# Performance work log

Measured on AMD Instinct MI355X. Metric: run time of the kernel, lower is better.

## Reference

```python
import jax, jax.numpy as jnp
import numpy as np

N_VARS = 4000
N_LITS = 2 * N_VARS
N_CLAUSES = 16000
N_CELLS = 48000
DIM = 128
N_ROUNDS = 16
N_PROBS = 8


def _mlp(x, w1, b1, w2, b2, w3, b3):
    x = jax.nn.relu(x @ w1.T + b1)
    x = jax.nn.relu(x @ w2.T + b2)
    return x @ w3.T + b3


def _lstm_step(x, h, c, wih, whh, bih, bhh):
    # PyTorch LSTM gate order: i, f, g, o
    gates = x @ wih.T + bih + h @ whh.T + bhh
    i, f, g, o = jnp.split(gates, 4, axis=-1)
    c = jax.nn.sigmoid(f) * c + jax.nn.sigmoid(i) * jnp.tanh(g)
    h = jax.nn.sigmoid(o) * jnp.tanh(c)
    return h, c


def setup_inputs() -> dict:
    key = jax.random.key(0)
    ks = iter(jax.random.split(key, 64))

    def p(shape, scale=0.05):
        return jax.random.normal(next(ks), shape, dtype=jnp.float32) * scale

    lit_idx = jax.random.randint(next(ks), (N_CELLS,), 0, N_LITS)
    cls_idx = jax.random.randint(next(ks), (N_CELLS,), 0, N_CLAUSES)
    L_unpack_indices = jnp.stack([lit_idx, cls_idx], axis=1)  # [n_cells, 2]

    return dict(
        L_unpack_indices=L_unpack_indices,
        n_vars=N_VARS, n_probs=N_PROBS, n_rounds=N_ROUNDS,
        L_init_w=p((DIM, 1)), L_init_b=p((DIM,)),
        C_init_w=p((DIM, 1)), C_init_b=p((DIM,)),
        Lmsg_w1=p((DIM, DIM)), Lmsg_b1=p((DIM,)),
        Lmsg_w2=p((DIM, DIM)), Lmsg_b2=p((DIM,)),
        Lmsg_w3=p((DIM, DIM)), Lmsg_b3=p((DIM,)),
        Cmsg_w1=p((DIM, DIM)), Cmsg_b1=p((DIM,)),
        Cmsg_w2=p((DIM, DIM)), Cmsg_b2=p((DIM,)),
        Cmsg_w3=p((DIM, DIM)), Cmsg_b3=p((DIM,)),
        Lvote_w1=p((DIM, DIM)), Lvote_b1=p((DIM,)),
        Lvote_w2=p((DIM, DIM)), Lvote_b2=p((DIM,)),
        Lvote_w3=p((1, DIM)), Lvote_b3=p((1,)),
        Lu_wih=p((4 * DIM, 2 * DIM)), Lu_whh=p((4 * DIM, DIM)),
        Lu_bih=p((4 * DIM,)), Lu_bhh=p((4 * DIM,)),
        Cu_wih=p((4 * DIM, DIM)), Cu_whh=p((4 * DIM, DIM)),
        Cu_bih=p((4 * DIM,)), Cu_bhh=p((4 * DIM,)),
    )


def reference(L_unpack_indices, n_vars, n_probs, n_rounds,
              L_init_w, L_init_b, C_init_w, C_init_b,
              Lmsg_w1, Lmsg_b1, Lmsg_w2, Lmsg_b2, Lmsg_w3, Lmsg_b3,
              Cmsg_w1, Cmsg_b1, Cmsg_w2, Cmsg_b2, Cmsg_w3, Cmsg_b3,
              Lvote_w1, Lvote_b1, Lvote_w2, Lvote_b2, Lvote_w3, Lvote_b3,
              Lu_wih, Lu_whh, Lu_bih, Lu_bhh,
              Cu_wih, Cu_whh, Cu_bih, Cu_bhh):
    n_lits = 2 * n_vars
    dim = L_init_b.shape[0]
    n_clauses = N_CLAUSES

    # densified literal-clause incidence matrix (matches torch.sparse -> to_dense)
    M = jnp.zeros((n_lits, n_clauses), jnp.float32).at[
        L_unpack_indices[:, 0], L_unpack_indices[:, 1]].add(1.0)

    # L_init/C_init applied to ts = ones(1)
    L0 = jnp.broadcast_to(L_init_w[:, 0] + L_init_b, (n_lits, dim))
    C0 = jnp.broadcast_to(C_init_w[:, 0] + C_init_b, (n_clauses, dim))
    carry0 = (L0, jnp.zeros((n_lits, dim), jnp.float32),
              C0, jnp.zeros((n_clauses, dim), jnp.float32))

    def round_fn(carry, _):
        Lh, Lc, Ch, Cc = carry
        L_pre = _mlp(Lh, Lmsg_w1, Lmsg_b1, Lmsg_w2, Lmsg_b2, Lmsg_w3, Lmsg_b3)
        LC_msg = M.T @ L_pre                      # [n_clauses, dim]
        Ch, Cc = _lstm_step(LC_msg, Ch, Cc, Cu_wih, Cu_whh, Cu_bih, Cu_bhh)
        C_pre = _mlp(Ch, Cmsg_w1, Cmsg_b1, Cmsg_w2, Cmsg_b2, Cmsg_w3, Cmsg_b3)
        CL_msg = M @ C_pre                        # [n_lits, dim]
        flipped = jnp.concatenate([Lh[n_vars:2 * n_vars], Lh[:n_vars]], axis=0)
        Lh, Lc = _lstm_step(jnp.concatenate([CL_msg, flipped], axis=1),
                            Lh, Lc, Lu_wih, Lu_whh, Lu_bih, Lu_bhh)
        return (Lh, Lc, Ch, Cc), None

    (Lh, _, _, _), _ = jax.lax.scan(round_fn, carry0, None, length=n_rounds)

    vote = _mlp(Lh, Lvote_w1, Lvote_b1, Lvote_w2, Lvote_b2, Lvote_w3, Lvote_b3)  # [n_lits, 1]
    vote_join = jnp.concatenate([vote[:n_vars], vote[n_vars:]], axis=1)          # [n_vars, 2]
    vote_join = vote_join.reshape(n_probs, -1)
    return jnp.mean(vote_join, axis=1)
```

## Files before the change

kernel.cpp:

```cpp
#include <hip/hip_runtime.h>
#include <cstdint>
#include <cstddef>

#define N_VARS   4000
#define N_LITS   8000
#define N_CLAUSES 16000
#define N_CELLS  48000
#define DIM      128
#define N_ROUNDS 16
#define N_PROBS  8

typedef __bf16 bf16x8 __attribute__((ext_vector_type(8)));
typedef float f32x4 __attribute__((ext_vector_type(4)));

__device__ inline unsigned short f2bf(float x) {
  unsigned int u = __float_as_uint(x);
  u += 0x7fffu + ((u >> 16) & 1u);
  return (unsigned short)(u >> 16);
}
__device__ inline float bflo(unsigned int v) { return __uint_as_float(v << 16); }
__device__ inline float bfhi(unsigned int v) { return __uint_as_float(v & 0xffff0000u); }
__device__ inline unsigned int pack2(float a, float b) {
  return (unsigned int)f2bf(a) | ((unsigned int)f2bf(b) << 16);
}
__device__ inline bf16x8 ld_frag(const unsigned short* p) {
  uint4 u = *reinterpret_cast<const uint4*>(p);
  return __builtin_bit_cast(bf16x8, u);
}
__device__ inline float fast_sigmoid(float x) { return 1.f / (1.f + __expf(-x)); }
__device__ inline float fast_tanh(float x) {
  float t = __expf(-2.f * x);
  return (1.f - t) / (1.f + t);
}


template<int KS, bool LIT>
__global__ __launch_bounds__(512, 4) void fused_round(
    const int* __restrict__ ptr, const int* __restrict__ col,
    const unsigned short* __restrict__ Tsrc,
    const unsigned short* hold, unsigned short* hnew,
    float* __restrict__ cst,
    const unsigned short* __restrict__ Wp, const float* __restrict__ bP,
    const unsigned short* __restrict__ Wm1, const float* __restrict__ bm1,
    const unsigned short* __restrict__ Wm2, const float* __restrict__ bm2,
    const unsigned short* __restrict__ Wm3, const float* __restrict__ bm3,
    unsigned short* __restrict__ Tout) {
  __shared__ __align__(16) unsigned short msg[32][136];
  __shared__ __align__(16) unsigned short hsA[32][136];
  __shared__ __align__(16) unsigned short hsF[LIT ? 32 : 1][136];
  __shared__ __align__(16) unsigned short xb[32][136];
  const int tid = threadIdx.x;
  const int w = tid >> 6, l = tid & 63;
  const int r = l & 15, kc = l >> 4;
  const int row0 = blockIdx.x * 32;
  const int flipoff = LIT ? ((row0 < N_VARS) ? N_VARS : -N_VARS) : 0;

  float s[16];
  {
    const int g8 = tid >> 3, gl = tid & 7;
    const int grow = g8 & 31, part = g8 >> 5;
    const int row = row0 + grow;
    const int b = ptr[row], e = ptr[row + 1];
#pragma unroll
    for (int q = 0; q < 16; ++q) s[q] = 0.f;
    int j = b + part;
    int c0 = (j < e) ? col[j] : 0;
    while (j < e) {
      const int jn = j + 2;
      const int c1 = (jn < e) ? col[jn] : 0;
      const unsigned short* src = &Tsrc[(size_t)c0 * 128 + gl * 16];
      const uint4 v0 = *reinterpret_cast<const uint4*>(src);
      const uint4 v1 = *reinterpret_cast<const uint4*>(src + 8);
      s[0]  += bflo(v0.x); s[1]  += bfhi(v0.x);
      s[2]  += bflo(v0.y); s[3]  += bfhi(v0.y);
      s[4]  += bflo(v0.z); s[5]  += bfhi(v0.z);
      s[6]  += bflo(v0.w); s[7]  += bfhi(v0.w);
      s[8]  += bflo(v1.x); s[9]  += bfhi(v1.x);
      s[10] += bflo(v1.y); s[11] += bfhi(v1.y);
      s[12] += bflo(v1.z); s[13] += bfhi(v1.z);
      s[14] += bflo(v1.w); s[15] += bfhi(v1.w);
      j = jn; c0 = c1;
    }
    if (part == 1) {
      uint4 o0, o1;
      o0.x = pack2(s[0], s[1]);  o0.y = pack2(s[2], s[3]);
      o0.z = pack2(s[4], s[5]);  o0.w = pack2(s[6], s[7]);
      o1.x = pack2(s[8], s[9]);  o1.y = pack2(s[10], s[11]);
      o1.z = pack2(s[12], s[13]); o1.w = pack2(s[14], s[15]);
      *reinterpret_cast<uint4*>(&msg[grow][gl * 16]) = o0;
      *reinterpret_cast<uint4*>(&msg[grow][gl * 16 + 8]) = o1;
    }
  }
  __syncthreads();

  {
    const int g8 = tid >> 3, gl = tid & 7;
    const int grow = g8 & 31, part = g8 >> 5;
    if (part == 0) {
      const uint4 m0 = *reinterpret_cast<const uint4*>(&msg[grow][gl * 16]);
      const uint4 m1 = *reinterpret_cast<const uint4*>(&msg[grow][gl * 16 + 8]);
      s[0]  += bflo(m0.x); s[1]  += bfhi(m0.x);
      s[2]  += bflo(m0.y); s[3]  += bfhi(m0.y);
      s[4]  += bflo(m0.z); s[5]  += bfhi(m0.z);
      s[6]  += bflo(m0.w); s[7]  += bfhi(m0.w);
      s[8]  += bflo(m1.x); s[9]  += bfhi(m1.x);
      s[10] += bflo(m1.y); s[11] += bfhi(m1.y);
      s[12] += bflo(m1.z); s[13] += bfhi(m1.z);
      s[14] += bflo(m1.w); s[15] += bfhi(m1.w);
      uint4 o0, o1;
      o0.x = pack2(s[0], s[1]);  o0.y = pack2(s[2], s[3]);
      o0.z = pack2(s[4], s[5]);  o0.w = pack2(s[6], s[7]);
      o1.x = pack2(s[8], s[9]);  o1.y = pack2(s[10], s[11]);
      o1.z = pack2(s[12], s[13]); o1.w = pack2(s[14], s[15]);
      *reinterpret_cast<uint4*>(&msg[grow][gl * 16]) = o0;
      *reinterpret_cast<uint4*>(&msg[grow][gl * 16 + 8]) = o1;
    } else {
      const int sidx = tid - 256;
#pragma unroll
      for (int q = 0; q < 2; ++q) {
        const int n = sidx + q * 256;
        const int rw = n >> 4, c8 = (n & 15) * 8;
        *reinterpret_cast<uint4*>(&hsA[rw][c8]) =
            *reinterpret_cast<const uint4*>(&hold[(size_t)(row0 + rw) * 128 + c8]);
        if (LIT)
          *reinterpret_cast<uint4*>(&hsF[rw][c8]) =
              *reinterpret_cast<const uint4*>(&hold[(size_t)(row0 + flipoff + rw) * 128 + c8]);
      }
    }
  }
  __syncthreads();

  f32x4 acc[2][4];
#pragma unroll
  for (int rg = 0; rg < 2; ++rg)
#pragma unroll
    for (int t = 0; t < 4; ++t) acc[rg][t] = (f32x4){0.f, 0.f, 0.f, 0.f};

#pragma unroll
  for (int ks = 0; ks < KS; ++ks) {
    bf16x8 bfr[2];
#pragma unroll
    for (int rg = 0; rg < 2; ++rg) {
      const int xr = rg * 16 + r;
      if (ks < 4)        bfr[rg] = ld_frag(&msg[xr][ks * 32 + kc * 8]);
      else if (!LIT)     bfr[rg] = ld_frag(&hsA[xr][(ks - 4) * 32 + kc * 8]);
      else if (ks < 8)   bfr[rg] = ld_frag(&hsF[xr][(ks - 4) * 32 + kc * 8]);
      else               bfr[rg] = ld_frag(&hsA[xr][(ks - 8) * 32 + kc * 8]);
    }
#pragma unroll
    for (int tt = 0; tt < 4; ++tt) {
      bf16x8 afr = ld_frag(&Wp[(size_t)(((w * KS + ks) * 4 + tt) * 64 + l) * 8]);
      acc[0][tt] = __builtin_amdgcn_mfma_f32_16x16x32_bf16(afr, bfr[0], acc[0][tt], 0, 0, 0);
      acc[1][tt] = __builtin_amdgcn_mfma_f32_16x16x32_bf16(afr, bfr[1], acc[1][tt], 0, 0, 0);
    }
  }
  __syncthreads();

  {
    const int d0 = w * 16 + kc * 4;
#pragma unroll
    for (int rg = 0; rg < 2; ++rg) {
      const int row = row0 + rg * 16 + r;
      const size_t cb = (size_t)row * 128 + d0;
      f32x4 cv = *reinterpret_cast<const f32x4*>(&cst[cb]);
      f32x4 cn4;
      unsigned int hp[2];
#pragma unroll
      for (int tt = 0; tt < 4; ++tt) {
        const float4 bb = *reinterpret_cast<const float4*>(&bP[w * 64 + tt * 16 + kc * 4]);
        float ig = acc[rg][tt][0] + bb.x;
        float fg = acc[rg][tt][1] + bb.y;
        float gg = acc[rg][tt][2] + bb.z;
        float og = acc[rg][tt][3] + bb.w;
        float cn = fast_sigmoid(fg) * cv[tt] + fast_sigmoid(ig) * fast_tanh(gg);
        float hv = fast_sigmoid(og) * fast_tanh(cn);
        cn4[tt] = cn;
        if (tt & 1) hp[tt >> 1] |= (unsigned int)f2bf(hv) << 16;
        else        hp[tt >> 1]  = (unsigned int)f2bf(hv);
      }
      *reinterpret_cast<f32x4*>(&cst[cb]) = cn4;
      uint2 hv2 = {hp[0], hp[1]};
      *reinterpret_cast<uint2*>(&hnew[cb]) = hv2;
      *reinterpret_cast<uint2*>(&hsA[rg * 16 + r][d0]) = hv2;
    }
  }
  __syncthreads();

  const int mrg = w >> 2;
  const int t0 = (w & 3) * 2;
  {
    f32x4 a2[2] = {(f32x4){0.f, 0.f, 0.f, 0.f}, (f32x4){0.f, 0.f, 0.f, 0.f}};
#pragma unroll
    for (int ks = 0; ks < 4; ++ks) {
      bf16x8 af = ld_frag(&hsA[mrg * 16 + r][ks * 32 + kc * 8]);
#pragma unroll
      for (int q = 0; q < 2; ++q) {
        bf16x8 bf = ld_frag(&Wm1[(size_t)(((t0 + q) * 4 + ks) * 64 + l) * 8]);
        a2[q] = __builtin_amdgcn_mfma_f32_16x16x32_bf16(af, bf, a2[q], 0, 0, 0);
      }
    }
#pragma unroll
    for (int q = 0; q < 2; ++q) {
      float bv = bm1[(t0 + q) * 16 + r];
#pragma unroll
      for (int j = 0; j < 4; ++j)
        xb[mrg * 16 + kc * 4 + j][(t0 + q) * 16 + r] = f2bf(fmaxf(a2[q][j] + bv, 0.f));
    }
  }
  __syncthreads();
  {
    f32x4 a2[2] = {(f32x4){0.f, 0.f, 0.f, 0.f}, (f32x4){0.f, 0.f, 0.f, 0.f}};
#pragma unroll
    for (int ks = 0; ks < 4; ++ks) {
      bf16x8 af = ld_frag(&xb[mrg * 16 + r][ks * 32 + kc * 8]);
#pragma unroll
      for (int q = 0; q < 2; ++q) {
        bf16x8 bf = ld_frag(&Wm2[(size_t)(((t0 + q) * 4 + ks) * 64 + l) * 8]);
        a2[q] = __builtin_amdgcn_mfma_f32_16x16x32_bf16(af, bf, a2[q], 0, 0, 0);
      }
    }
#pragma unroll
    for (int q = 0; q < 2; ++q) {
      float bv = bm2[(t0 + q) * 16 + r];
#pragma unroll
      for (int j = 0; j < 4; ++j)
        msg[mrg * 16 + kc * 4 + j][(t0 + q) * 16 + r] = f2bf(fmaxf(a2[q][j] + bv, 0.f));
    }
  }
  __syncthreads();
  {
    f32x4 a2[2] = {(f32x4){0.f, 0.f, 0.f, 0.f}, (f32x4){0.f, 0.f, 0.f, 0.f}};
#pragma unroll
    for (int ks = 0; ks < 4; ++ks) {
      bf16x8 af = ld_frag(&msg[mrg * 16 + r][ks * 32 + kc * 8]);
#pragma unroll
      for (int q = 0; q < 2; ++q) {
        bf16x8 bf = ld_frag(&Wm3[(size_t)(((t0 + q) * 4 + ks) * 64 + l) * 8]);
        a2[q] = __builtin_amdgcn_mfma_f32_16x16x32_bf16(af, bf, a2[q], 0, 0, 0);
      }
    }
#pragma unroll
    for (int q = 0; q < 2; ++q) {
      float bv = bm3[(t0 + q) * 16 + r];
#pragma unroll
      for (int j = 0; j < 4; ++j)
        Tout[(size_t)(row0 + mrg * 16 + kc * 4 + j) * 128 + (t0 + q) * 16 + r] =
            f2bf(a2[q][j] + bv);
    }
  }
}

__global__ __launch_bounds__(256) void fused_mlp3(
    const unsigned short* __restrict__ A,
    const unsigned short* __restrict__ W1, const float* __restrict__ b1,
    const unsigned short* __restrict__ W2, const float* __restrict__ b2,
    const unsigned short* __restrict__ W3, const float* __restrict__ b3,
    unsigned short* __restrict__ out) {
  __shared__ __align__(16) unsigned short xbuf[2][4][16][136];
  const int w = threadIdx.x >> 6, l = threadIdx.x & 63;
  const int r = l & 15, kc = l >> 4;
  const int row0 = blockIdx.x * 64 + w * 16;

  f32x4 acc[8];
#pragma unroll
  for (int t = 0; t < 8; ++t) acc[t] = (f32x4){0.f, 0.f, 0.f, 0.f};
#pragma unroll
  for (int ks = 0; ks < 4; ++ks) {
    bf16x8 a = ld_frag(&A[(size_t)(row0 + r) * 128 + ks * 32 + kc * 8]);
#pragma unroll
    for (int t = 0; t < 8; ++t) {
      bf16x8 b = ld_frag(&W1[(size_t)((t * 4 + ks) * 64 + l) * 8]);
      acc[t] = __builtin_amdgcn_mfma_f32_16x16x32_bf16(a, b, acc[t], 0, 0, 0);
    }
  }
#pragma unroll
  for (int t = 0; t < 8; ++t) {
    float bv = b1[t * 16 + r];
#pragma unroll
    for (int j = 0; j < 4; ++j)
      xbuf[0][w][kc * 4 + j][t * 16 + r] = f2bf(fmaxf(acc[t][j] + bv, 0.f));
  }
// ... 113 lines not shown
__global__ void pack8_kernel(const float* s0, const float* s1, const float* s2, const float* s3,
                             const float* s4, const float* s5, const float* s6, const float* s7,
                             unsigned short* d0, unsigned short* d1, unsigned short* d2,
                             unsigned short* d3, unsigned short* d4, unsigned short* d5,
                             unsigned short* d6, unsigned short* d7) {
  int i = blockIdx.x * 256 + threadIdx.x;
  const float* s; unsigned short* d;
  switch (blockIdx.y) {
    case 0: s = s0; d = d0; break;
    case 1: s = s1; d = d1; break;
    case 2: s = s2; d = d2; break;
    case 3: s = s3; d = d3; break;
    case 4: s = s4; d = d4; break;
    case 5: s = s5; d = d5; break;
    case 6: s = s6; d = d6; break;
    default: s = s7; d = d7; break;
  }
  int np = i >> 7, k = i & 127;
  int tt = np >> 4, r = np & 15;
  int ks = k >> 5, kcf = (k >> 3) & 3, e = k & 7;
  int dst = (((tt * 4 + ks) * 64) + kcf * 16 + r) * 8 + e;
  d[dst] = f2bf(s[i]);
}

template<int KIH>
__global__ void pack_gates_kernel(const float* __restrict__ wih, const float* __restrict__ whh,
                                  const float* __restrict__ bih, const float* __restrict__ bhh,
                                  unsigned short* __restrict__ Wp, float* __restrict__ bP) {
  constexpr int K = KIH + 128;
  constexpr int KS = K / 32;
  int idx = blockIdx.x * 256 + threadIdx.x;
  if (idx >= 512 * K) return;
  int np = idx / K, k = idx % K;
  int gt = np & 3;
  int d = ((np >> 6) << 4) + (((np >> 2) & 3) << 2) + ((np >> 4) & 3);
  int orig = gt * 128 + d;
  float v = (k < KIH) ? wih[(size_t)orig * KIH + k] : whh[(size_t)orig * 128 + (k - KIH)];
  int w = np >> 6, tt = (np >> 4) & 3, r = np & 15;
  int ks = k >> 5, kcf = (k >> 3) & 3, e = k & 7;
  size_t dst = ((size_t)((w * KS + ks) * 4 + tt) * 64 + kcf * 16 + r) * 8 + e;
  Wp[dst] = f2bf(v);
  if (k == 0) bP[np] = bih[orig] + bhh[orig];
}

__global__ void count_kernel(const int* __restrict__ uidx,
                             int* __restrict__ lit_cnt, int* __restrict__ cls_cnt) {
  int i = blockIdx.x * 256 + threadIdx.x;
  if (i < N_CELLS) {
    atomicAdd(&lit_cnt[uidx[2 * i]], 1);
    atomicAdd(&cls_cnt[uidx[2 * i + 1]], 1);
  }
}

__global__ void scan_kernel(const int* __restrict__ cnt, int* __restrict__ ptr, int n) {
  __shared__ int part[1024];
  __shared__ int total;
  int t = threadIdx.x;
  int chunk = (n + 1023) >> 10;
  int lo = t * chunk, hi = min(lo + chunk, n);
  int s = 0;
  for (int i = lo; i < hi; ++i) s += cnt[i];
  part[t] = s;
  __syncthreads();
  if (t == 0) {
    int acc = 0;
    for (int i = 0; i < 1024; ++i) { int v = part[i]; part[i] = acc; acc += v; }
    total = acc;
  }
  __syncthreads();
  int acc = part[t];
  for (int i = lo; i < hi; ++i) { ptr[i] = acc; acc += cnt[i]; }
  if (t == 0) ptr[n] = total;
}
// ... 80 lines not shown
  unsigned short* wV2  = (unsigned short*)alloc(DIM * DIM * 2);
  int* lit_cnt  = (int*)alloc(N_LITS * 4);
  int* cls_cnt  = (int*)alloc(N_CLAUSES * 4);
  int* lit_fill = (int*)alloc(N_LITS * 4);
  int* cls_fill = (int*)alloc(N_CLAUSES * 4);
  int* lit_ptr  = (int*)alloc((N_LITS + 1) * 4);
  int* cls_ptr  = (int*)alloc((N_CLAUSES + 1) * 4);
  int* lit_col  = (int*)alloc(N_CELLS * 4);
  int* cls_col  = (int*)alloc(N_CELLS * 4);
  if (off > ws_size) return;

  hipMemsetAsync(lit_cnt, 0, (char*)lit_ptr - (char*)lit_cnt, stream);
  count_kernel<<<(N_CELLS + 255) / 256, 256, 0, stream>>>(uidx, lit_cnt, cls_cnt);
  scan_kernel<<<1, 1024, 0, stream>>>(lit_cnt, lit_ptr, N_LITS);
  scan_kernel<<<1, 1024, 0, stream>>>(cls_cnt, cls_ptr, N_CLAUSES);
  scatter_kernel<<<(N_CELLS + 255) / 256, 256, 0, stream>>>(
      uidx, lit_ptr, cls_ptr, lit_fill, cls_fill, lit_col, cls_col);

  init_state_kernel<<<(N_CLAUSES * DIM + 255) / 256, 256, 0, stream>>>(
      L_init_w, L_init_b, C_init_w, C_init_b, LhA, Lc, Ch, Cc);
  pack_gates_kernel<256><<<(512 * 384 + 255) / 256, 256, 0, stream>>>(
      Lu_wih, Lu_whh, Lu_bih, Lu_bhh, WLp, bL);
  pack_gates_kernel<128><<<(512 * 256 + 255) / 256, 256, 0, stream>>>(
      Cu_wih, Cu_whh, Cu_bih, Cu_bhh, WCp, bC);
  dim3 cgrid(DIM * DIM / 256, 8);
  pack8_kernel<<<cgrid, 256, 0, stream>>>(
      Lmsg_w1, Lmsg_w2, Lmsg_w3, Cmsg_w1, Cmsg_w2, Cmsg_w3, Lvote_w1, Lvote_w2,
      wLm1, wLm2, wLm3, wCm1, wCm2, wCm3, wV1, wV2);

  fused_mlp3<<<N_LITS / 64, 256, 0, stream>>>(
      LhA, wLm1, Lmsg_b1, wLm2, Lmsg_b2, wLm3, Lmsg_b3, TL);

  for (int r = 0; r < N_ROUNDS; ++r) {
    fused_round<8, false><<<N_CLAUSES / 32, 512, 0, stream>>>(
        cls_ptr, cls_col, TL, Ch, Ch, Cc, WCp, bC,
        wCm1, Cmsg_b1, wCm2, Cmsg_b2, wCm3, Cmsg_b3, TC);
    const unsigned short* lold = (r & 1) ? LhB : LhA;
    unsigned short* lnew = (r & 1) ? LhA : LhB;
    fused_round<12, true><<<N_LITS / 32, 512, 0, stream>>>(
        lit_ptr, lit_col, TC, lold, lnew, Lc, WLp, bL,
        wLm1, Lmsg_b1, wLm2, Lmsg_b2, wLm3, Lmsg_b3, TL);
  }

  fused_vote<<<N_LITS / 64, 256, 0, stream>>>(
      LhA, wV1, Lvote_b1, wV2, Lvote_b2, Lvote_w3, Lvote_b3, vote);
  prob_mean_kernel<<<N_PROBS, 256, 0, stream>>>(vote, out);
}
```

Baseline: 715.7 us.

## Double fused_round block to 1024 threads and prefetch hidden state early

Each per-round fused kernel now uses 1024 threads (16 waves) per 32-row tile instead of 512. The gather uses 16 lanes per row with 8 elements each, each wave computes half as many gate tiles, and each MLP wave produces one output tile. The gate weight packing is reordered to match. The old hidden-state rows are loaded into registers at kernel start so their latency overlaps the sparse gather. This is meant to raise parallelism and latency hiding, at the cost of scalar (non-vectorised) cell-state and hidden writes, more waves per block and an extra barrier.

```diff
diff --git a/kernel.cpp b/kernel.cpp
--- a/kernel.cpp
+++ b/kernel.cpp
@@ -35,7 +35,7 @@
 
 
 template<int KS, bool LIT>
-__global__ __launch_bounds__(512, 4) void fused_round(
+__global__ __launch_bounds__(1024, 8) void fused_round(
     const int* __restrict__ ptr, const int* __restrict__ col,
     const unsigned short* __restrict__ Tsrc,
     const unsigned short* hold, unsigned short* hnew,
@@ -53,88 +53,74 @@
   const int w = tid >> 6, l = tid & 63;
   const int r = l & 15, kc = l >> 4;
   const int row0 = blockIdx.x * 32;
-  const int flipoff = LIT ? ((row0 < N_VARS) ? N_VARS : -N_VARS) : 0;
-
-  float s[16];
+
+  uint4 stA, stF;
+  if (tid >= 512) {
+    const int sidx = tid - 512;
+    const int rw = sidx >> 4, c8 = (sidx & 15) * 8;
+    stA = *reinterpret_cast<const uint4*>(&hold[(size_t)(row0 + rw) * 128 + c8]);
+    if (LIT) {
+      const int gr = row0 + rw;
+      const int fr = (gr < N_VARS) ? gr + N_VARS : gr - N_VARS;
+      stF = *reinterpret_cast<const uint4*>(&hold[(size_t)fr * 128 + c8]);
+    }
+  }
+
+  float s[8];
   {
-    const int g8 = tid >> 3, gl = tid & 7;
-    const int grow = g8 & 31, part = g8 >> 5;
+    const int g16 = tid >> 4, gl = tid & 15;
+    const int grow = g16 & 31, part = g16 >> 5;
     const int row = row0 + grow;
     const int b = ptr[row], e = ptr[row + 1];
 #pragma unroll
-    for (int q = 0; q < 16; ++q) s[q] = 0.f;
+    for (int q = 0; q < 8; ++q) s[q] = 0.f;
     int j = b + part;
     int c0 = (j < e) ? col[j] : 0;
     while (j < e) {
       const int jn = j + 2;
       const int c1 = (jn < e) ? col[jn] : 0;
-      const unsigned short* src = &Tsrc[(size_t)c0 * 128 + gl * 16];
-      const uint4 v0 = *reinterpret_cast<const uint4*>(src);
-      const uint4 v1 = *reinterpret_cast<const uint4*>(src + 8);
-      s[0]  += bflo(v0.x); s[1]  += bfhi(v0.x);
-      s[2]  += bflo(v0.y); s[3]  += bfhi(v0.y);
-      s[4]  += bflo(v0.z); s[5]  += bfhi(v0.z);
-      s[6]  += bflo(v0.w); s[7]  += bfhi(v0.w);
-      s[8]  += bflo(v1.x); s[9]  += bfhi(v1.x);
-      s[10] += bflo(v1.y); s[11] += bfhi(v1.y);
-      s[12] += bflo(v1.z); s[13] += bfhi(v1.z);
-      s[14] += bflo(v1.w); s[15] += bfhi(v1.w);
+      const uint4 v = *reinterpret_cast<const uint4*>(&Tsrc[(size_t)c0 * 128 + gl * 8]);
+      s[0] += bflo(v.x); s[1] += bfhi(v.x);
+      s[2] += bflo(v.y); s[3] += bfhi(v.y);
+      s[4] += bflo(v.z); s[5] += bfhi(v.z);
+      s[6] += bflo(v.w); s[7] += bfhi(v.w);
       j = jn; c0 = c1;
     }
     if (part == 1) {
-      uint4 o0, o1;
-      o0.x = pack2(s[0], s[1]);  o0.y = pack2(s[2], s[3]);
-      o0.z = pack2(s[4], s[5]);  o0.w = pack2(s[6], s[7]);
-      o1.x = pack2(s[8], s[9]);  o1.y = pack2(s[10], s[11]);
-      o1.z = pack2(s[12], s[13]); o1.w = pack2(s[14], s[15]);
-      *reinterpret_cast<uint4*>(&msg[grow][gl * 16]) = o0;
-      *reinterpret_cast<uint4*>(&msg[grow][gl * 16 + 8]) = o1;
+      uint4 o;
+      o.x = pack2(s[0], s[1]); o.y = pack2(s[2], s[3]);
+      o.z = pack2(s[4], s[5]); o.w = pack2(s[6], s[7]);
+      *reinterpret_cast<uint4*>(&msg[grow][gl * 8]) = o;
     }
   }
   __syncthreads();
 
   {
-    const int g8 = tid >> 3, gl = tid & 7;
-    const int grow = g8 & 31, part = g8 >> 5;
+    const int g16 = tid >> 4, gl = tid & 15;
+    const int grow = g16 & 31, part = g16 >> 5;
     if (part == 0) {
-      const uint4 m0 = *reinterpret_cast<const uint4*>(&msg[grow][gl * 16]);
-      const uint4 m1 = *reinterpret_cast<const uint4*>(&msg[grow][gl * 16 + 8]);
-      s[0]  += bflo(m0.x); s[1]  += bfhi(m0.x);
-      s[2]  += bflo(m0.y); s[3]  += bfhi(m0.y);
-      s[4]  += bflo(m0.z); s[5]  += bfhi(m0.z);
-      s[6]  += bflo(m0.w); s[7]  += bfhi(m0.w);
-      s[8]  += bflo(m1.x); s[9]  += bfhi(m1.x);
-      s[10] += bflo(m1.y); s[11] += bfhi(m1.y);
-      s[12] += bflo(m1.z); s[13] += bfhi(m1.z);
-      s[14] += bflo(m1.w); s[15] += bfhi(m1.w);
-      uint4 o0, o1;
-      o0.x = pack2(s[0], s[1]);  o0.y = pack2(s[2], s[3]);
-      o0.z = pack2(s[4], s[5]);  o0.w = pack2(s[6], s[7]);
-      o1.x = pack2(s[8], s[9]);  o1.y = pack2(s[10], s[11]);
-      o1.z = pack2(s[12], s[13]); o1.w = pack2(s[14], s[15]);
-      *reinterpret_cast<uint4*>(&msg[grow][gl * 16]) = o0;
-      *reinterpret_cast<uint4*>(&msg[grow][gl * 16 + 8]) = o1;
+      const uint4 m = *reinterpret_cast<const uint4*>(&msg[grow][gl * 8]);
+      uint4 o;
+      o.x = pack2(s[0] + bflo(m.x), s[1] + bfhi(m.x));
+      o.y = pack2(s[2] + bflo(m.y), s[3] + bfhi(m.y));
+      o.z = pack2(s[4] + bflo(m.z), s[5] + bfhi(m.z));
+      o.w = pack2(s[6] + bflo(m.w), s[7] + bfhi(m.w));
+      *reinterpret_cast<uint4*>(&msg[grow][gl * 8]) = o;
     } else {
-      const int sidx = tid - 256;
-#pragma unroll
-      for (int q = 0; q < 2; ++q) {
-        const int n = sidx + q * 256;
-        const int rw = n >> 4, c8 = (n & 15) * 8;
-        *reinterpret_cast<uint4*>(&hsA[rw][c8]) =
-            *reinterpret_cast<const uint4*>(&hold[(size_t)(row0 + rw) * 128 + c8]);
-        if (LIT)
-          *reinterpret_cast<uint4*>(&hsF[rw][c8]) =
-              *reinterpret_cast<const uint4*>(&hold[(size_t)(row0 + flipoff + rw) * 128 + c8]);
-      }
-    }
-  }
-  __syncthreads();
-
-  f32x4 acc[2][4];
+      const int sidx = tid - 512;
+      const int rw = sidx >> 4, c8 = (sidx & 15) * 8;
+      *reinterpret_cast<uint4*>(&hsA[rw][c8]) = stA;
+      if (LIT)
+        *reinterpret_cast<uint4*>(&hsF[rw][c8]) = stF;
+    }
+  }
+  __syncthreads();
+
+  f32x4 acc[2][2];
 #pragma unroll
   for (int rg = 0; rg < 2; ++rg)
 #pragma unroll
-    for (int t = 0; t < 4; ++t) acc[rg][t] = (f32x4){0.f, 0.f, 0.f, 0.f};
+    for (int t = 0; t < 2; ++t) acc[rg][t] = (f32x4){0.f, 0.f, 0.f, 0.f};
 
 #pragma unroll
   for (int ks = 0; ks < KS; ++ks) {
@@ -148,8 +134,8 @@
       else               bfr[rg] = ld_frag(&hsA[xr][(ks - 8) * 32 + kc * 8]);
     }
 #pragma unroll
-    for (int tt = 0; tt < 4; ++tt) {
-      bf16x8 afr = ld_frag(&Wp[(size_t)(((w * KS + ks) * 4 + tt) * 64 + l) * 8]);
+    for (int tt = 0; tt < 2; ++tt) {
+      bf16x8 afr = ld_frag(&Wp[(size_t)(((w * KS + ks) * 2 + tt) * 64 + l) * 8]);
       acc[0][tt] = __builtin_amdgcn_mfma_f32_16x16x32_bf16(afr, bfr[0], acc[0][tt], 0, 0, 0);
       acc[1][tt] = __builtin_amdgcn_mfma_f32_16x16x32_bf16(afr, bfr[1], acc[1][tt], 0, 0, 0);
     }
@@ -157,96 +143,74 @@
   __syncthreads();
 
   {
-    const int d0 = w * 16 + kc * 4;
 #pragma unroll
     for (int rg = 0; rg < 2; ++rg) {
       const int row = row0 + rg * 16 + r;
-      const size_t cb = (size_t)row * 128 + d0;
-      f32x4 cv = *reinterpret_cast<const f32x4*>(&cst[cb]);
-      f32x4 cn4;
-      unsigned int hp[2];
-#pragma unroll
-      for (int tt = 0; tt < 4; ++tt) {
-        const float4 bb = *reinterpret_cast<const float4*>(&bP[w * 64 + tt * 16 + kc * 4]);
+#pragma unroll
+      for (int tt = 0; tt < 2; ++tt) {
+        const int d = w * 8 + tt * 4 + kc;
+        const size_t cb = (size_t)row * 128 + d;
+        const float4 bb = *reinterpret_cast<const float4*>(&bP[w * 32 + tt * 16 + kc * 4]);
         float ig = acc[rg][tt][0] + bb.x;
         float fg = acc[rg][tt][1] + bb.y;
         float gg = acc[rg][tt][2] + bb.z;
         float og = acc[rg][tt][3] + bb.w;
-        float cn = fast_sigmoid(fg) * cv[tt] + fast_sigmoid(ig) * fast_tanh(gg);
+        float cp = cst[cb];
+        float cn = fast_sigmoid(fg) * cp + fast_sigmoid(ig) * fast_tanh(gg);
         float hv = fast_sigmoid(og) * fast_tanh(cn);
-        cn4[tt] = cn;
-        if (tt & 1) hp[tt >> 1] |= (unsigned int)f2bf(hv) << 16;
-        else        hp[tt >> 1]  = (unsigned int)f2bf(hv);
+        cst[cb] = cn;
+        unsigned short hb16 = f2bf(hv);
+        hnew[cb] = hb16;
+        hsA[rg * 16 + r][d] = hb16;
       }
-      *reinterpret_cast<f32x4*>(&cst[cb]) = cn4;
-      uint2 hv2 = {hp[0], hp[1]};
-      *reinterpret_cast<uint2*>(&hnew[cb]) = hv2;
-      *reinterpret_cast<uint2*>(&hsA[rg * 16 + r][d0]) = hv2;
-    }
-  }
-  __syncthreads();
-
-  const int mrg = w >> 2;
-  const int t0 = (w & 3) * 2;
+    }
+  }
+  __syncthreads();
+
+  const int mrg = w >> 3;
+  const int t0 = w & 7;
   {
-    f32x4 a2[2] = {(f32x4){0.f, 0.f, 0.f, 0.f}, (f32x4){0.f, 0.f, 0.f, 0.f}};
+    f32x4 a2 = (f32x4){0.f, 0.f, 0.f, 0.f};
 #pragma unroll
     for (int ks = 0; ks < 4; ++ks) {
       bf16x8 af = ld_frag(&hsA[mrg * 16 + r][ks * 32 + kc * 8]);
-#pragma unroll
-      for (int q = 0; q < 2; ++q) {
-        bf16x8 bf = ld_frag(&Wm1[(size_t)(((t0 + q) * 4 + ks) * 64 + l) * 8]);
-        a2[q] = __builtin_amdgcn_mfma_f32_16x16x32_bf16(af, bf, a2[q], 0, 0, 0);
-      }
-    }
-#pragma unroll
-    for (int q = 0; q < 2; ++q) {
-      float bv = bm1[(t0 + q) * 16 + r];
-#pragma unroll
-      for (int j = 0; j < 4; ++j)
-        xb[mrg * 16 + kc * 4 + j][(t0 + q) * 16 + r] = f2bf(fmaxf(a2[q][j] + bv, 0.f));
-    }
+      bf16x8 bf = ld_frag(&Wm1[(size_t)((t0 * 4 + ks) * 64 + l) * 8]);
+      a2 = __builtin_amdgcn_mfma_f32_16x16x32_bf16(af, bf, a2, 0, 0, 0);
+    }
+    float bv = bm1[t0 * 16 + r];
+#pragma unroll
+    for (int j = 0; j < 4; ++j)
+      xb[mrg * 16 + kc * 4 + j][t0 * 16 + r] = f2bf(fmaxf(a2[j] + bv, 0.f));
   }
   __syncthreads();
   {
-    f32x4 a2[2] = {(f32x4){0.f, 0.f, 0.f, 0.f}, (f32x4){0.f, 0.f, 0.f, 0.f}};
+    f32x4 a2 = (f32x4){0.f, 0.f, 0.f, 0.f};
 #pragma unroll
     for (int ks = 0; ks < 4; ++ks) {
       bf16x8 af = ld_frag(&xb[mrg * 16 + r][ks * 32 + kc * 8]);
-#pragma unroll
-      for (int q = 0; q < 2; ++q) {
-        bf16x8 bf = ld_frag(&Wm2[(size_t)(((t0 + q) * 4 + ks) * 64 + l) * 8]);
-        a2[q] = __builtin_amdgcn_mfma_f32_16x16x32_bf16(af, bf, a2[q], 0, 0, 0);
-      }
-    }
-#pragma unroll
-    for (int q = 0; q < 2; ++q) {
-      float bv = bm2[(t0 + q) * 16 + r];
-#pragma unroll
-      for (int j = 0; j < 4; ++j)
-        msg[mrg * 16 + kc * 4 + j][(t0 + q) * 16 + r] = f2bf(fmaxf(a2[q][j] + bv, 0.f));
-    }
+      bf16x8 bf = ld_frag(&Wm2[(size_t)((t0 * 4 + ks) * 64 + l) * 8]);
+      a2 = __builtin_amdgcn_mfma_f32_16x16x32_bf16(af, bf, a2, 0, 0, 0);
+    }
+    float bv = bm2[t0 * 16 + r];
+    __syncthreads();
+#pragma unroll
+    for (int j = 0; j < 4; ++j)
+      msg[mrg * 16 + kc * 4 + j][t0 * 16 + r] = f2bf(fmaxf(a2[j] + bv, 0.f));
   }
   __syncthreads();
   {
-    f32x4 a2[2] = {(f32x4){0.f, 0.f, 0.f, 0.f}, (f32x4){0.f, 0.f, 0.f, 0.f}};
+    f32x4 a2 = (f32x4){0.f, 0.f, 0.f, 0.f};
 #pragma unroll
     for (int ks = 0; ks < 4; ++ks) {
       bf16x8 af = ld_frag(&msg[mrg * 16 + r][ks * 32 + kc * 8]);
-#pragma unroll
-      for (int q = 0; q < 2; ++q) {
-        bf16x8 bf = ld_frag(&Wm3[(size_t)(((t0 + q) * 4 + ks) * 64 + l) * 8]);
-        a2[q] = __builtin_amdgcn_mfma_f32_16x16x32_bf16(af, bf, a2[q], 0, 0, 0);
-      }
-    }
-#pragma unroll
-    for (int q = 0; q < 2; ++q) {
-      float bv = bm3[(t0 + q) * 16 + r];
-#pragma unroll
-      for (int j = 0; j < 4; ++j)
-        Tout[(size_t)(row0 + mrg * 16 + kc * 4 + j) * 128 + (t0 + q) * 16 + r] =
-            f2bf(a2[q][j] + bv);
-    }
+      bf16x8 bf = ld_frag(&Wm3[(size_t)((t0 * 4 + ks) * 64 + l) * 8]);
+      a2 = __builtin_amdgcn_mfma_f32_16x16x32_bf16(af, bf, a2, 0, 0, 0);
+    }
+    float bv = bm3[t0 * 16 + r];
+#pragma unroll
+    for (int j = 0; j < 4; ++j)
+      Tout[(size_t)(row0 + mrg * 16 + kc * 4 + j) * 128 + t0 * 16 + r] =
+          f2bf(a2[j] + bv);
   }
 }
 
@@ -427,12 +391,12 @@
   if (idx >= 512 * K) return;
   int np = idx / K, k = idx % K;
   int gt = np & 3;
-  int d = ((np >> 6) << 4) + (((np >> 2) & 3) << 2) + ((np >> 4) & 3);
+  int d = ((np >> 5) << 3) + (((np >> 4) & 1) << 2) + ((np >> 2) & 3);
   int orig = gt * 128 + d;
   float v = (k < KIH) ? wih[(size_t)orig * KIH + k] : whh[(size_t)orig * 128 + (k - KIH)];
-  int w = np >> 6, tt = (np >> 4) & 3, r = np & 15;
+  int w = np >> 5, tt = (np >> 4) & 1, rr = np & 15;
   int ks = k >> 5, kcf = (k >> 3) & 3, e = k & 7;
-  size_t dst = ((size_t)((w * KS + ks) * 4 + tt) * 64 + kcf * 16 + r) * 8 + e;
+  size_t dst = ((size_t)((w * KS + ks) * 2 + tt) * 64 + kcf * 16 + rr) * 8 + e;
   Wp[dst] = f2bf(v);
   if (k == 0) bP[np] = bih[orig] + bhh[orig];
 }
@@ -579,12 +543,12 @@
       LhA, wLm1, Lmsg_b1, wLm2, Lmsg_b2, wLm3, Lmsg_b3, TL);
 
   for (int r = 0; r < N_ROUNDS; ++r) {
-    fused_round<8, false><<<N_CLAUSES / 32, 512, 0, stream>>>(
+    fused_round<8, false><<<N_CLAUSES / 32, 1024, 0, stream>>>(
         cls_ptr, cls_col, TL, Ch, Ch, Cc, WCp, bC,
         wCm1, Cmsg_b1, wCm2, Cmsg_b2, wCm3, Cmsg_b3, TC);
     const unsigned short* lold = (r & 1) ? LhB : LhA;
     unsigned short* lnew = (r & 1) ? LhA : LhB;
-    fused_round<12, true><<<N_LITS / 32, 512, 0, stream>>>(
+    fused_round<12, true><<<N_LITS / 32, 1024, 0, stream>>>(
         lit_ptr, lit_col, TC, lold, lnew, Lc, WLp, bL,
         wLm1, Lmsg_b1, wLm2, Lmsg_b2, wLm3, Lmsg_b3, TL);
   }
```

Measured after the change: 818.4 us. 14.4% more time.

## Halve literal-round tile to 16 rows and prefetch hidden state before gather

Applied to the files above, without the earlier changes.

Adds an RG template parameter so the literal-side round kernel processes 16 rows per block, doubling the block count to 500 for better CU coverage. The gather is split into four partial sums per row, reduced through a small shared buffer. The old hidden state and its flipped counterpart are loaded into registers before the sparse gather so their latency overlaps with it. The trade-off is half the MFMA work per weight fragment load in the literal kernel, so weight traffic per row roughly doubles.

```diff
diff --git a/kernel.cpp b/kernel.cpp
--- a/kernel.cpp
+++ b/kernel.cpp
@@ -34,7 +34,7 @@
 }
 
 
-template<int KS, bool LIT>
+template<int KS, int RG, bool LIT>
 __global__ __launch_bounds__(512, 4) void fused_round(
     const int* __restrict__ ptr, const int* __restrict__ col,
     const unsigned short* __restrict__ Tsrc,
@@ -45,20 +45,39 @@
     const unsigned short* __restrict__ Wm2, const float* __restrict__ bm2,
     const unsigned short* __restrict__ Wm3, const float* __restrict__ bm3,
     unsigned short* __restrict__ Tout) {
-  __shared__ __align__(16) unsigned short msg[32][136];
-  __shared__ __align__(16) unsigned short hsA[32][136];
-  __shared__ __align__(16) unsigned short hsF[LIT ? 32 : 1][136];
-  __shared__ __align__(16) unsigned short xb[32][136];
+  constexpr int ROWS = RG * 16;
+  __shared__ __align__(16) unsigned short msg[ROWS][136];
+  __shared__ __align__(16) unsigned short hsA[ROWS][136];
+  __shared__ __align__(16) unsigned short hsF[LIT ? ROWS : 1][136];
+  __shared__ __align__(16) unsigned short xb[ROWS][136];
+  __shared__ __align__(16) unsigned short pmsg[RG == 1 ? 3 : 1][RG == 1 ? 16 : 1][136];
   const int tid = threadIdx.x;
   const int w = tid >> 6, l = tid & 63;
   const int r = l & 15, kc = l >> 4;
-  const int row0 = blockIdx.x * 32;
-  const int flipoff = LIT ? ((row0 < N_VARS) ? N_VARS : -N_VARS) : 0;
+  const int row0 = blockIdx.x * ROWS;
+
+  uint4 stA[2], stF[2];
+  if (tid >= 256) {
+    const int sidx = tid - 256;
+#pragma unroll
+    for (int q = 0; q < RG; ++q) {
+      const int n = sidx + q * 256;
+      const int rw = n >> 4, c8 = (n & 15) * 8;
+      stA[q] = *reinterpret_cast<const uint4*>(&hold[(size_t)(row0 + rw) * 128 + c8]);
+      if (LIT) {
+        const int gr = row0 + rw;
+        const int fr = (gr < N_VARS) ? gr + N_VARS : gr - N_VARS;
+        stF[q] = *reinterpret_cast<const uint4*>(&hold[(size_t)fr * 128 + c8]);
+      }
+    }
+  }
 
   float s[16];
   {
     const int g8 = tid >> 3, gl = tid & 7;
-    const int grow = g8 & 31, part = g8 >> 5;
+    const int grow = (RG == 2) ? (g8 & 31) : (g8 & 15);
+    const int part = (RG == 2) ? (g8 >> 5) : (g8 >> 4);
+    constexpr int NPART = (RG == 2) ? 2 : 4;
     const int row = row0 + grow;
     const int b = ptr[row], e = ptr[row + 1];
 #pragma unroll
@@ -66,7 +85,7 @@
     int j = b + part;
     int c0 = (j < e) ? col[j] : 0;
     while (j < e) {
-      const int jn = j + 2;
+      const int jn = j + NPART;
       const int c1 = (jn < e) ? col[jn] : 0;
       const unsigned short* src = &Tsrc[(size_t)c0 * 128 + gl * 16];
       const uint4 v0 = *reinterpret_cast<const uint4*>(src);
@@ -81,7 +100,51 @@
       s[14] += bflo(v1.w); s[15] += bfhi(v1.w);
       j = jn; c0 = c1;
     }
-    if (part == 1) {
+    if (part > 0) {
+      uint4 o0, o1;
+      o0.x = pack2(s[0], s[1]);  o0.y = pack2(s[2], s[3]);
+      o0.z = pack2(s[4], s[5]);  o0.w = pack2(s[6], s[7]);
+      o1.x = pack2(s[8], s[9]);  o1.y = pack2(s[10], s[11]);
+      o1.z = pack2(s[12], s[13]); o1.w = pack2(s[14], s[15]);
+      unsigned short* dst = (RG == 2) ? &msg[grow][gl * 16]
+                                      : &pmsg[part - 1][grow][gl * 16];
+      *reinterpret_cast<uint4*>(dst) = o0;
+      *reinterpret_cast<uint4*>(dst + 8) = o1;
+    }
+  }
+  __syncthreads();
+
+  {
+    const int g8 = tid >> 3, gl = tid & 7;
+    const int grow = (RG == 2) ? (g8 & 31) : (g8 & 15);
+    const int part = (RG == 2) ? (g8 >> 5) : (g8 >> 4);
+    if (part == 0) {
+      if (RG == 2) {
+        const uint4 m0 = *reinterpret_cast<const uint4*>(&msg[grow][gl * 16]);
+        const uint4 m1 = *reinterpret_cast<const uint4*>(&msg[grow][gl * 16 + 8]);
+        s[0]  += bflo(m0.x); s[1]  += bfhi(m0.x);
+        s[2]  += bflo(m0.y); s[3]  += bfhi(m0.y);
+        s[4]  += bflo(m0.z); s[5]  += bfhi(m0.z);
+        s[6]  += bflo(m0.w); s[7]  += bfhi(m0.w);
+        s[8]  += bflo(m1.x); s[9]  += bfhi(m1.x);
+        s[10] += bflo(m1.y); s[11] += bfhi(m1.y);
+        s[12] += bflo(m1.z); s[13] += bfhi(m1.z);
+        s[14] += bflo(m1.w); s[15] += bfhi(m1.w);
+      } else {
+#pragma unroll
+        for (int p = 0; p < 3; ++p) {
+          const uint4 m0 = *reinterpret_cast<const uint4*>(&pmsg[p][grow][gl * 16]);
+          const uint4 m1 = *reinterpret_cast<const uint4*>(&pmsg[p][grow][gl * 16 + 8]);
+          s[0]  += bflo(m0.x); s[1]  += bfhi(m0.x);
+          s[2]  += bflo(m0.y); s[3]  += bfhi(m0.y);
+          s[4]  += bflo(m0.z); s[5]  += bfhi(m0.z);
+          s[6]  += bflo(m0.w); s[7]  += bfhi(m0.w);
+          s[8]  += bflo(m1.x); s[9]  += bfhi(m1.x);
+          s[10] += bflo(m1.y); s[11] += bfhi(m1.y);
+          s[12] += bflo(m1.z); s[13] += bfhi(m1.z);
+          s[14] += bflo(m1.w); s[15] += bfhi(m1.w);
+        }
+      }
       uint4 o0, o1;
       o0.x = pack2(s[0], s[1]);  o0.y = pack2(s[2], s[3]);
       o0.z = pack2(s[4], s[5]);  o0.w = pack2(s[6], s[7]);
@@ -89,58 +152,31 @@
       o1.z = pack2(s[12], s[13]); o1.w = pack2(s[14], s[15]);
       *reinterpret_cast<uint4*>(&msg[grow][gl * 16]) = o0;
       *reinterpret_cast<uint4*>(&msg[grow][gl * 16 + 8]) = o1;
-    }
-  }
-  __syncthreads();
-
-  {
-    const int g8 = tid >> 3, gl = tid & 7;
-    const int grow = g8 & 31, part = g8 >> 5;
-    if (part == 0) {
-      const uint4 m0 = *reinterpret_cast<const uint4*>(&msg[grow][gl * 16]);
-      const uint4 m1 = *reinterpret_cast<const uint4*>(&msg[grow][gl * 16 + 8]);
-      s[0]  += bflo(m0.x); s[1]  += bfhi(m0.x);
-      s[2]  += bflo(m0.y); s[3]  += bfhi(m0.y);
-      s[4]  += bflo(m0.z); s[5]  += bfhi(m0.z);
-      s[6]  += bflo(m0.w); s[7]  += bfhi(m0.w);
-      s[8]  += bflo(m1.x); s[9]  += bfhi(m1.x);
-      s[10] += bflo(m1.y); s[11] += bfhi(m1.y);
-      s[12] += bflo(m1.z); s[13] += bfhi(m1.z);
-      s[14] += bflo(m1.w); s[15] += bfhi(m1.w);
-      uint4 o0, o1;
-      o0.x = pack2(s[0], s[1]);  o0.y = pack2(s[2], s[3]);
-      o0.z = pack2(s[4], s[5]);  o0.w = pack2(s[6], s[7]);
-      o1.x = pack2(s[8], s[9]);  o1.y = pack2(s[10], s[11]);
-      o1.z = pack2(s[12], s[13]); o1.w = pack2(s[14], s[15]);
-      *reinterpret_cast<uint4*>(&msg[grow][gl * 16]) = o0;
-      *reinterpret_cast<uint4*>(&msg[grow][gl * 16 + 8]) = o1;
-    } else {
+    } else if (tid >= 256) {
       const int sidx = tid - 256;
 #pragma unroll
-      for (int q = 0; q < 2; ++q) {
+      for (int q = 0; q < RG; ++q) {
         const int n = sidx + q * 256;
         const int rw = n >> 4, c8 = (n & 15) * 8;
-        *reinterpret_cast<uint4*>(&hsA[rw][c8]) =
-            *reinterpret_cast<const uint4*>(&hold[(size_t)(row0 + rw) * 128 + c8]);
+        *reinterpret_cast<uint4*>(&hsA[rw][c8]) = stA[q];
         if (LIT)
-          *reinterpret_cast<uint4*>(&hsF[rw][c8]) =
-              *reinterpret_cast<const uint4*>(&hold[(size_t)(row0 + flipoff + rw) * 128 + c8]);
+          *reinterpret_cast<uint4*>(&hsF[rw][c8]) = stF[q];
       }
     }
   }
   __syncthreads();
 
-  f32x4 acc[2][4];
-#pragma unroll
-  for (int rg = 0; rg < 2; ++rg)
+  f32x4 acc[RG][4];
+#pragma unroll
+  for (int rg = 0; rg < RG; ++rg)
 #pragma unroll
     for (int t = 0; t < 4; ++t) acc[rg][t] = (f32x4){0.f, 0.f, 0.f, 0.f};
 
 #pragma unroll
   for (int ks = 0; ks < KS; ++ks) {
-    bf16x8 bfr[2];
-#pragma unroll
-    for (int rg = 0; rg < 2; ++rg) {
+    bf16x8 bfr[RG];
+#pragma unroll
+    for (int rg = 0; rg < RG; ++rg) {
       const int xr = rg * 16 + r;
       if (ks < 4)        bfr[rg] = ld_frag(&msg[xr][ks * 32 + kc * 8]);
       else if (!LIT)     bfr[rg] = ld_frag(&hsA[xr][(ks - 4) * 32 + kc * 8]);
@@ -150,8 +186,9 @@
 #pragma unroll
     for (int tt = 0; tt < 4; ++tt) {
       bf16x8 afr = ld_frag(&Wp[(size_t)(((w * KS + ks) * 4 + tt) * 64 + l) * 8]);
-      acc[0][tt] = __builtin_amdgcn_mfma_f32_16x16x32_bf16(afr, bfr[0], acc[0][tt], 0, 0, 0);
-      acc[1][tt] = __builtin_amdgcn_mfma_f32_16x16x32_bf16(afr, bfr[1], acc[1][tt], 0, 0, 0);
+#pragma unroll
+      for (int rg = 0; rg < RG; ++rg)
+        acc[rg][tt] = __builtin_amdgcn_mfma_f32_16x16x32_bf16(afr, bfr[rg], acc[rg][tt], 0, 0, 0);
     }
   }
   __syncthreads();
@@ -159,7 +196,7 @@
   {
     const int d0 = w * 16 + kc * 4;
 #pragma unroll
-    for (int rg = 0; rg < 2; ++rg) {
+    for (int rg = 0; rg < RG; ++rg) {
       const int row = row0 + rg * 16 + r;
       const size_t cb = (size_t)row * 128 + d0;
       f32x4 cv = *reinterpret_cast<const f32x4*>(&cst[cb]);
@@ -186,21 +223,24 @@
   }
   __syncthreads();
 
-  const int mrg = w >> 2;
-  const int t0 = (w & 3) * 2;
+  constexpr int TPW = (RG == 2) ? 2 : 1;
+  const int mrg = (RG == 2) ? (w >> 2) : 0;
+  const int t0 = (RG == 2) ? ((w & 3) * 2) : w;
   {
-    f32x4 a2[2] = {(f32x4){0.f, 0.f, 0.f, 0.f}, (f32x4){0.f, 0.f, 0.f, 0.f}};
+    f32x4 a2[TPW];
+#pragma unroll
+    for (int q = 0; q < TPW; ++q) a2[q] = (f32x4){0.f, 0.f, 0.f, 0.f};
 #pragma unroll
     for (int ks = 0; ks < 4; ++ks) {
       bf16x8 af = ld_frag(&hsA[mrg * 16 + r][ks * 32 + kc * 8]);
 #pragma unroll
-      for (int q = 0; q < 2; ++q) {
+      for (int q = 0; q < TPW; ++q) {
         bf16x8 bf = ld_frag(&Wm1[(size_t)(((t0 + q) * 4 + ks) * 64 + l) * 8]);
         a2[q] = __builtin_amdgcn_mfma_f32_16x16x32_bf16(af, bf, a2[q], 0, 0, 0);
       }
     }
 #pragma unroll
-    for (int q = 0; q < 2; ++q) {
+    for (int q = 0; q < TPW; ++q) {
       float bv = bm1[(t0 + q) * 16 + r];
 #pragma unroll
       for (int j = 0; j < 4; ++j)
@@ -209,18 +249,20 @@
   }
   __syncthreads();
   {
-    f32x4 a2[2] = {(f32x4){0.f, 0.f, 0.f, 0.f}, (f32x4){0.f, 0.f, 0.f, 0.f}};
+    f32x4 a2[TPW];
+#pragma unroll
+    for (int q = 0; q < TPW; ++q) a2[q] = (f32x4){0.f, 0.f, 0.f, 0.f};
 #pragma unroll
     for (int ks = 0; ks < 4; ++ks) {
       bf16x8 af = ld_frag(&xb[mrg * 16 + r][ks * 32 + kc * 8]);
 #pragma unroll
-      for (int q = 0; q < 2; ++q) {
+      for (int q = 0; q < TPW; ++q) {
         bf16x8 bf = ld_frag(&Wm2[(size_t)(((t0 + q) * 4 + ks) * 64 + l) * 8]);
         a2[q] = __builtin_amdgcn_mfma_f32_16x16x32_bf16(af, bf, a2[q], 0, 0, 0);
       }
     }
 #pragma unroll
-    for (int q = 0; q < 2; ++q) {
+    for (int q = 0; q < TPW; ++q) {
       float bv = bm2[(t0 + q) * 16 + r];
 #pragma unroll
       for (int j = 0; j < 4; ++j)
@@ -229,18 +271,20 @@
   }
   __syncthreads();
   {
-    f32x4 a2[2] = {(f32x4){0.f, 0.f, 0.f, 0.f}, (f32x4){0.f, 0.f, 0.f, 0.f}};
+    f32x4 a2[TPW];
+#pragma unroll
+    for (int q = 0; q < TPW; ++q) a2[q] = (f32x4){0.f, 0.f, 0.f, 0.f};
 #pragma unroll
     for (int ks = 0; ks < 4; ++ks) {
       bf16x8 af = ld_frag(&msg[mrg * 16 + r][ks * 32 + kc * 8]);
 #pragma unroll
-      for (int q = 0; q < 2; ++q) {
+      for (int q = 0; q < TPW; ++q) {
         bf16x8 bf = ld_frag(&Wm3[(size_t)(((t0 + q) * 4 + ks) * 64 + l) * 8]);
         a2[q] = __builtin_amdgcn_mfma_f32_16x16x32_bf16(af, bf, a2[q], 0, 0, 0);
       }
     }
 #pragma unroll
-    for (int q = 0; q < 2; ++q) {
+    for (int q = 0; q < TPW; ++q) {
       float bv = bm3[(t0 + q) * 16 + r];
 #pragma unroll
       for (int j = 0; j < 4; ++j)
@@ -430,9 +474,9 @@
   int d = ((np >> 6) << 4) + (((np >> 2) & 3) << 2) + ((np >> 4) & 3);
   int orig = gt * 128 + d;
   float v = (k < KIH) ? wih[(size_t)orig * KIH + k] : whh[(size_t)orig * 128 + (k - KIH)];
-  int w = np >> 6, tt = (np >> 4) & 3, r = np & 15;
+  int w = np >> 6, tt = (np >> 4) & 3, rr = np & 15;
   int ks = k >> 5, kcf = (k >> 3) & 3, e = k & 7;
-  size_t dst = ((size_t)((w * KS + ks) * 4 + tt) * 64 + kcf * 16 + r) * 8 + e;
+  size_t dst = ((size_t)((w * KS + ks) * 4 + tt) * 64 + kcf * 16 + rr) * 8 + e;
   Wp[dst] = f2bf(v);
   if (k == 0) bP[np] = bih[orig] + bhh[orig];
 }
@@ -579,12 +623,12 @@
       LhA, wLm1, Lmsg_b1, wLm2, Lmsg_b2, wLm3, Lmsg_b3, TL);
 
   for (int r = 0; r < N_ROUNDS; ++r) {
-    fused_round<8, false><<<N_CLAUSES / 32, 512, 0, stream>>>(
+    fused_round<8, 2, false><<<N_CLAUSES / 32, 512, 0, stream>>>(
         cls_ptr, cls_col, TL, Ch, Ch, Cc, WCp, bC,
         wCm1, Cmsg_b1, wCm2, Cmsg_b2, wCm3, Cmsg_b3, TC);
     const unsigned short* lold = (r & 1) ? LhB : LhA;
     unsigned short* lnew = (r & 1) ? LhA : LhB;
-    fused_round<12, true><<<N_LITS / 32, 512, 0, stream>>>(
+    fused_round<12, 1, true><<<N_LITS / 16, 512, 0, stream>>>(
         lit_ptr, lit_col, TC, lold, lnew, Lc, WLp, bL,
         wLm1, Lmsg_b1, wLm2, Lmsg_b2, wLm3, Lmsg_b3, TL);
   }
```

Measured after the change: 715.4 us. About the same (-0.0%).

## Retile LSTM gate GEMM per wave and prefetch hidden state before gather

Applied to the files above, without the earlier changes.

Each wave now computes 8 gate tiles (128 gate outputs) for one 16-row half instead of 4 tiles for both row halves. The gate weight packing is reordered so each thread owns 8 contiguous hidden dims, which gives 16-byte cell-state and h stores. The hidden-state and flipped-state global loads are issued into registers before the sparse gather loop, so their latency overlaps the gather. Each wave now reads twice as much weight data from global memory per block but only one B fragment per k-step, and register pressure rises.

```diff
diff --git a/kernel.cpp b/kernel.cpp
--- a/kernel.cpp
+++ b/kernel.cpp
@@ -53,7 +53,22 @@
   const int w = tid >> 6, l = tid & 63;
   const int r = l & 15, kc = l >> 4;
   const int row0 = blockIdx.x * 32;
-  const int flipoff = LIT ? ((row0 < N_VARS) ? N_VARS : -N_VARS) : 0;
+
+  uint4 stA[2], stF[2];
+  if (tid >= 256) {
+    const int sidx = tid - 256;
+#pragma unroll
+    for (int q = 0; q < 2; ++q) {
+      const int n = sidx + q * 256;
+      const int rw = n >> 4, c8 = (n & 15) * 8;
+      stA[q] = *reinterpret_cast<const uint4*>(&hold[(size_t)(row0 + rw) * 128 + c8]);
+      if (LIT) {
+        const int gr = row0 + rw;
+        const int fr = (gr < N_VARS) ? gr + N_VARS : gr - N_VARS;
+        stF[q] = *reinterpret_cast<const uint4*>(&hold[(size_t)fr * 128 + c8]);
+      }
+    }
+  }
 
   float s[16];
   {
@@ -114,75 +129,71 @@
       o1.z = pack2(s[12], s[13]); o1.w = pack2(s[14], s[15]);
       *reinterpret_cast<uint4*>(&msg[grow][gl * 16]) = o0;
       *reinterpret_cast<uint4*>(&msg[grow][gl * 16 + 8]) = o1;
-    } else {
+    } else if (tid >= 256) {
       const int sidx = tid - 256;
 #pragma unroll
       for (int q = 0; q < 2; ++q) {
         const int n = sidx + q * 256;
         const int rw = n >> 4, c8 = (n & 15) * 8;
-        *reinterpret_cast<uint4*>(&hsA[rw][c8]) =
-            *reinterpret_cast<const uint4*>(&hold[(size_t)(row0 + rw) * 128 + c8]);
+        *reinterpret_cast<uint4*>(&hsA[rw][c8]) = stA[q];
         if (LIT)
-          *reinterpret_cast<uint4*>(&hsF[rw][c8]) =
-              *reinterpret_cast<const uint4*>(&hold[(size_t)(row0 + flipoff + rw) * 128 + c8]);
+          *reinterpret_cast<uint4*>(&hsF[rw][c8]) = stF[q];
       }
     }
   }
   __syncthreads();
 
-  f32x4 acc[2][4];
-#pragma unroll
-  for (int rg = 0; rg < 2; ++rg)
-#pragma unroll
-    for (int t = 0; t < 4; ++t) acc[rg][t] = (f32x4){0.f, 0.f, 0.f, 0.f};
+  const int sl = w & 3;
+  const int rh = w >> 2;
+  f32x4 acc[8];
+#pragma unroll
+  for (int t = 0; t < 8; ++t) acc[t] = (f32x4){0.f, 0.f, 0.f, 0.f};
 
 #pragma unroll
   for (int ks = 0; ks < KS; ++ks) {
-    bf16x8 bfr[2];
-#pragma unroll
-    for (int rg = 0; rg < 2; ++rg) {
-      const int xr = rg * 16 + r;
-      if (ks < 4)        bfr[rg] = ld_frag(&msg[xr][ks * 32 + kc * 8]);
-      else if (!LIT)     bfr[rg] = ld_frag(&hsA[xr][(ks - 4) * 32 + kc * 8]);
-      else if (ks < 8)   bfr[rg] = ld_frag(&hsF[xr][(ks - 4) * 32 + kc * 8]);
-      else               bfr[rg] = ld_frag(&hsA[xr][(ks - 8) * 32 + kc * 8]);
-    }
-#pragma unroll
-    for (int tt = 0; tt < 4; ++tt) {
-      bf16x8 afr = ld_frag(&Wp[(size_t)(((w * KS + ks) * 4 + tt) * 64 + l) * 8]);
-      acc[0][tt] = __builtin_amdgcn_mfma_f32_16x16x32_bf16(afr, bfr[0], acc[0][tt], 0, 0, 0);
-      acc[1][tt] = __builtin_amdgcn_mfma_f32_16x16x32_bf16(afr, bfr[1], acc[1][tt], 0, 0, 0);
+    bf16x8 bfr;
+    {
+      const int xr = rh * 16 + r;
+      if (ks < 4)        bfr = ld_frag(&msg[xr][ks * 32 + kc * 8]);
+      else if (!LIT)     bfr = ld_frag(&hsA[xr][(ks - 4) * 32 + kc * 8]);
+      else if (ks < 8)   bfr = ld_frag(&hsF[xr][(ks - 4) * 32 + kc * 8]);
+      else               bfr = ld_frag(&hsA[xr][(ks - 8) * 32 + kc * 8]);
+    }
+#pragma unroll
+    for (int tt = 0; tt < 8; ++tt) {
+      bf16x8 afr = ld_frag(&Wp[(size_t)(((sl * KS + ks) * 8 + tt) * 64 + l) * 8]);
+      acc[tt] = __builtin_amdgcn_mfma_f32_16x16x32_bf16(afr, bfr, acc[tt], 0, 0, 0);
     }
   }
   __syncthreads();
 
   {
-    const int d0 = w * 16 + kc * 4;
-#pragma unroll
-    for (int rg = 0; rg < 2; ++rg) {
-      const int row = row0 + rg * 16 + r;
-      const size_t cb = (size_t)row * 128 + d0;
-      f32x4 cv = *reinterpret_cast<const f32x4*>(&cst[cb]);
-      f32x4 cn4;
-      unsigned int hp[2];
-#pragma unroll
-      for (int tt = 0; tt < 4; ++tt) {
-        const float4 bb = *reinterpret_cast<const float4*>(&bP[w * 64 + tt * 16 + kc * 4]);
-        float ig = acc[rg][tt][0] + bb.x;
-        float fg = acc[rg][tt][1] + bb.y;
-        float gg = acc[rg][tt][2] + bb.z;
-        float og = acc[rg][tt][3] + bb.w;
-        float cn = fast_sigmoid(fg) * cv[tt] + fast_sigmoid(ig) * fast_tanh(gg);
-        float hv = fast_sigmoid(og) * fast_tanh(cn);
-        cn4[tt] = cn;
-        if (tt & 1) hp[tt >> 1] |= (unsigned int)f2bf(hv) << 16;
-        else        hp[tt >> 1]  = (unsigned int)f2bf(hv);
-      }
-      *reinterpret_cast<f32x4*>(&cst[cb]) = cn4;
-      uint2 hv2 = {hp[0], hp[1]};
-      *reinterpret_cast<uint2*>(&hnew[cb]) = hv2;
-      *reinterpret_cast<uint2*>(&hsA[rg * 16 + r][d0]) = hv2;
-    }
+    const int row = row0 + rh * 16 + r;
+    const int d0 = sl * 32 + kc * 8;
+    const size_t cb = (size_t)row * 128 + d0;
+    f32x4 cv0 = *reinterpret_cast<const f32x4*>(&cst[cb]);
+    f32x4 cv1 = *reinterpret_cast<const f32x4*>(&cst[cb + 4]);
+    f32x4 n0, n1;
+    unsigned int hp[4];
+#pragma unroll
+    for (int tt = 0; tt < 8; ++tt) {
+      const float4 bb = *reinterpret_cast<const float4*>(&bP[sl * 128 + tt * 16 + kc * 4]);
+      float ig = acc[tt][0] + bb.x;
+      float fg = acc[tt][1] + bb.y;
+      float gg = acc[tt][2] + bb.z;
+      float og = acc[tt][3] + bb.w;
+      float cp = (tt < 4) ? cv0[tt] : cv1[tt - 4];
+      float cn = fast_sigmoid(fg) * cp + fast_sigmoid(ig) * fast_tanh(gg);
+      float hv = fast_sigmoid(og) * fast_tanh(cn);
+      if (tt < 4) n0[tt] = cn; else n1[tt - 4] = cn;
+      if (tt & 1) hp[tt >> 1] |= (unsigned int)f2bf(hv) << 16;
+      else        hp[tt >> 1]  = (unsigned int)f2bf(hv);
+    }
+    *reinterpret_cast<f32x4*>(&cst[cb]) = n0;
+    *reinterpret_cast<f32x4*>(&cst[cb + 4]) = n1;
+    uint4 hv4 = {hp[0], hp[1], hp[2], hp[3]};
+    *reinterpret_cast<uint4*>(&hnew[cb]) = hv4;
+    *reinterpret_cast<uint4*>(&hsA[rh * 16 + r][d0]) = hv4;
   }
   __syncthreads();
 
@@ -426,13 +437,12 @@
   int idx = blockIdx.x * 256 + threadIdx.x;
   if (idx >= 512 * K) return;
   int np = idx / K, k = idx % K;
-  int gt = np & 3;
-  int d = ((np >> 6) << 4) + (((np >> 2) & 3) << 2) + ((np >> 4) & 3);
+  int sl = np >> 7, tt = (np >> 4) & 7, kcp = (np >> 2) & 3, gt = np & 3;
+  int d = sl * 32 + kcp * 8 + tt;
   int orig = gt * 128 + d;
   float v = (k < KIH) ? wih[(size_t)orig * KIH + k] : whh[(size_t)orig * 128 + (k - KIH)];
-  int w = np >> 6, tt = (np >> 4) & 3, r = np & 15;
   int ks = k >> 5, kcf = (k >> 3) & 3, e = k & 7;
-  size_t dst = ((size_t)((w * KS + ks) * 4 + tt) * 64 + kcf * 16 + r) * 8 + e;
+  size_t dst = ((size_t)((sl * KS + ks) * 8 + tt) * 64 + kcf * 16 + (np & 15)) * 8 + e;
   Wp[dst] = f2bf(v);
   if (k == 0) bP[np] = bih[orig] + bhh[orig];
 }
```

Result: slower. 863.1 us (+20.6%).
